# Optimization experiments

Measured on AMD Instinct MI355X. Metric: run time of the kernel, lower is better.

## Reference

```python
import jax, jax.numpy as jnp
import numpy as np

NUM_HEADS = 8
HEAD_DIM = 64
HIDDEN = 512
ROPE_THETA = 500000.0


def _make_rope(seq_len, head_dim, theta):
    inv_freq = 1.0 / (theta ** (np.arange(0, head_dim, 2, dtype=np.float32) / head_dim))
    t = np.arange(seq_len, dtype=np.float32)
    freqs = np.outer(t, inv_freq)                  # [S, hd/2]
    emb = np.concatenate([freqs, freqs], axis=-1)  # [S, hd]
    return jnp.asarray(np.cos(emb)), jnp.asarray(np.sin(emb))


def setup_inputs() -> dict:
    key = jax.random.key(0)
    ks = jax.random.split(key, 5)
    B, S, H = 1, 4096, HIDDEN
    num_registers = 32
    hidden_states = jax.random.normal(ks[0], (B, S, H), dtype=jnp.float32)
    scale = 0.02
    Wq = jax.random.normal(ks[1], (H, H), dtype=jnp.float32) * scale
    Wk = jax.random.normal(ks[2], (H, H), dtype=jnp.float32) * scale
    Wv = jax.random.normal(ks[3], (H, H), dtype=jnp.float32) * scale
    Wo = jax.random.normal(ks[4], (H, H), dtype=jnp.float32) * scale
    cos, sin = _make_rope(S - num_registers, HEAD_DIM, ROPE_THETA)
    return {"hidden_states": hidden_states, "Wq": Wq, "Wk": Wk, "Wv": Wv,
            "Wo": Wo, "cos": cos, "sin": sin, "num_registers": num_registers}


def _rotate_half(x):
    x1, x2 = jnp.split(x, 2, axis=-1)
    return jnp.concatenate([-x2, x1], axis=-1)


def _apply_rope(q, k, cos, sin):
    # cos/sin: [S_real, hd] broadcast over [B, H, S_real, hd]
    cos = cos[None, None]
    sin = sin[None, None]
    return q * cos + _rotate_half(q) * sin, k * cos + _rotate_half(k) * sin


def reference(hidden_states, Wq, Wk, Wv, Wo, cos, sin, num_registers):
    B, S, _ = hidden_states.shape
    def proj(W):
        # torch Linear: x @ W.T -> [B, S, H] -> [B, nh, S, hd]
        y = jnp.einsum('bsh,oh->bso', hidden_states, W)
        return y.reshape(B, S, NUM_HEADS, HEAD_DIM).transpose(0, 2, 1, 3)
    q, k, v = proj(Wq), proj(Wk), proj(Wv)

    if num_registers > 0:
        q_reg, q_real = q[:, :, :num_registers], q[:, :, num_registers:]
        k_reg, k_real = k[:, :, :num_registers], k[:, :, num_registers:]
        q_real, k_real = _apply_rope(q_real, k_real, cos, sin)
        q = jnp.concatenate([q_reg, q_real], axis=2)
        k = jnp.concatenate([k_reg, k_real], axis=2)
    else:
        q, k = _apply_rope(q, k, cos, sin)

    scale = 1.0 / jnp.sqrt(jnp.float32(HEAD_DIM))
    scores = jnp.einsum('bhqd,bhkd->bhqk', q, k) * scale  # [B, nh, S, S]
    causal = jnp.tril(jnp.ones((S, S), dtype=bool))
    scores = jnp.where(causal[None, None], scores, jnp.float32(-1e30))
    attn = jax.nn.softmax(scores, axis=-1)
    out = jnp.einsum('bhqk,bhkd->bhqd', attn, v)
    out = out.transpose(0, 2, 1, 3).reshape(B, S, HIDDEN)
    return jnp.einsum('bsh,oh->bso', out, Wo)
```

## Files before the change

### kernel.cpp

```cpp
#include <hip/hip_runtime.h>
#include <cstdint>
#include <cstddef>

#define S_LEN 4096
#define HID   512
#define NHEAD 8
#define HD    64
#define SCALE_LOG2E 0.1803368801111204f

typedef __bf16 bf16;
typedef __bf16 bf16x8 __attribute__((ext_vector_type(8)));
typedef __bf16 bf16x4 __attribute__((ext_vector_type(4)));
typedef float  f32x4  __attribute__((ext_vector_type(4)));
typedef unsigned uint4v __attribute__((ext_vector_type(4)));

__global__ __launch_bounds__(256) void cvt_in(
    const float* __restrict__ hs, const float* __restrict__ wq,
    const float* __restrict__ wk, const float* __restrict__ wv,
    const float* __restrict__ wo,
    bf16* __restrict__ xb, bf16* __restrict__ wqb, bf16* __restrict__ wkb,
    bf16* __restrict__ wvb, bf16* __restrict__ wob)
{
    int e = (blockIdx.x * 256 + threadIdx.x) * 4;
    const float* s; bf16* d; int o;
    if (e < 2 * 1024 * 1024) { s = hs; d = xb; o = e; }
    else {
        int t = e - 2 * 1024 * 1024;
        int wi = t >> 18;
        o = t & ((1 << 18) - 1);
        s = (wi == 0) ? wq : (wi == 1) ? wk : (wi == 2) ? wv : wo;
        d = (wi == 0) ? wqb : (wi == 1) ? wkb : (wi == 2) ? wvb : wob;
    }
    const float4 v = *(const float4*)(s + o);
    bf16x4 ob;
    ob[0] = (bf16)v.x; ob[1] = (bf16)v.y; ob[2] = (bf16)v.z; ob[3] = (bf16)v.w;
    *(bf16x4*)(d + o) = ob;
}

__global__ __launch_bounds__(256) void gemm_qkv(
    const bf16* __restrict__ Xb,
    const bf16* __restrict__ W0, const bf16* __restrict__ W1, const bf16* __restrict__ W2,
    const float* __restrict__ cosT, const float* __restrict__ sinT,
    const int* __restrict__ nregp,
    bf16* __restrict__ Qh, bf16* __restrict__ Kh, bf16* __restrict__ Vt)
{
    const int z = blockIdx.z;
    const bf16* W = (z == 0) ? W0 : (z == 1 ? W1 : W2);
    const int m0 = blockIdx.y * 64, n0 = blockIdx.x * 128;
    __shared__ bf16 lA[64][8][8];
    __shared__ bf16 lB[128][8][8];
    __shared__ bf16 scratch[64][136];
    const int tid = threadIdx.x;
    const int lane = tid & 63, w = tid >> 6;
    const int l16 = lane & 15, lc = lane >> 4, l7 = lane & 7;
    const int wm = (w & 1) * 32, wn = (w >> 1) * 64;
    f32x4 acc[2][4] = {};

    for (int k0 = 0; k0 < HID; k0 += 64) {
        __syncthreads();
#pragma unroll
        for (int i = 0; i < 2; i++) {
            int uu = tid + 256 * i;
            int m = uu >> 3, c = uu & 7;
            *(bf16x8*)(&lA[m][c ^ (m & 7)][0]) =
                *(const bf16x8*)(Xb + (size_t)(m0 + m) * HID + k0 + 8 * c);
        }
#pragma unroll
        for (int i = 0; i < 4; i++) {
            int uu = tid + 256 * i;
            int m = uu >> 3, c = uu & 7;
            *(bf16x8*)(&lB[m][c ^ (m & 7)][0]) =
                *(const bf16x8*)(W + (size_t)(n0 + m) * HID + k0 + 8 * c);
        }
        __syncthreads();
#pragma unroll
        for (int ks = 0; ks < 2; ks++) {
            bf16x8 af[2], bfr[4];
#pragma unroll
            for (int i = 0; i < 2; i++)
                af[i]  = *(const bf16x8*)(&lA[wm + 16 * i + l16][(4 * ks + lc) ^ l7][0]);
#pragma unroll
            for (int j = 0; j < 4; j++)
                bfr[j] = *(const bf16x8*)(&lB[wn + 16 * j + l16][(4 * ks + lc) ^ l7][0]);
#pragma unroll
            for (int i = 0; i < 2; i++)
#pragma unroll
                for (int j = 0; j < 4; j++)
                    acc[i][j] = __builtin_amdgcn_mfma_f32_16x16x32_bf16(
                        af[i], bfr[j], acc[i][j], 0, 0, 0);
        }
    }

    if (z == 2) {
        const int h = (n0 + wn) >> 6;
#pragma unroll
        for (int i = 0; i < 2; i++) {
            const int s0r = m0 + wm + 16 * i + 4 * lc;
#pragma unroll
            for (int j = 0; j < 4; j++) {
                const int dl = 16 * j + l16;
                bf16x4 o;
#pragma unroll
                for (int r = 0; r < 4; r++) o[r] = (bf16)acc[i][j][r];
                *(bf16x4*)(Vt + ((size_t)(h * HD + dl)) * S_LEN + s0r) = o;
            }
        }
    } else {
        const int nreg = *nregp;
        bf16* dst = (z == 0) ? Qh : Kh;
#pragma unroll
        for (int i = 0; i < 2; i++) {
            const int sl0 = wm + 16 * i + 4 * lc;
#pragma unroll
            for (int r = 0; r < 4; r++) {
                const int s = m0 + sl0 + r;
                float c0 = 1.f, sn0 = 0.f, c1 = 1.f, sn1 = 0.f;
                if (s >= nreg) {
                    const int p = s - nreg;
                    c0  = cosT[(size_t)p * HD + l16];
                    sn0 = sinT[(size_t)p * HD + l16];
                    c1  = cosT[(size_t)p * HD + 16 + l16];
                    sn1 = sinT[(size_t)p * HD + 16 + l16];
                }
                const float x0 = acc[i][0][r], x1 = acc[i][1][r];
                const float x2 = acc[i][2][r], x3 = acc[i][3][r];
                bf16* row = &scratch[sl0 + r][wn];
                row[l16]      = (bf16)(x0 * c0 - x2 * sn0);
                row[l16 + 16] = (bf16)(x1 * c1 - x3 * sn1);
                row[l16 + 32] = (bf16)(x2 * c0 + x0 * sn0);
                row[l16 + 48] = (bf16)(x3 * c1 + x1 * sn1);
            }
        }
        __syncthreads();
        const int h0 = n0 >> 6;
#pragma unroll
        for (int i = 0; i < 4; i++) {
            int u = tid + 256 * i;
            int row = u >> 4, c = u & 15;
            bf16x8 val = *(const bf16x8*)(&scratch[row][c * 8]);
            *(bf16x8*)(dst + ((size_t)(h0 + (c >> 3)) * S_LEN + m0 + row) * HD +
                       (c & 7) * 8) = val;
        }
    }
}

__global__ __launch_bounds__(256) void gemm_out(
    const bf16* __restrict__ X, const bf16* __restrict__ Wb,
    float* __restrict__ Y)
{
    const int m0 = blockIdx.y * 64, n0 = blockIdx.x * 64;
    __shared__ bf16 lA[64][8][8];
    __shared__ bf16 lB[64][8][8];
    const int tid = threadIdx.x;
    const int lane = tid & 63, w = tid >> 6;
    const int l16 = lane & 15, lc = lane >> 4, l7 = lane & 7;
    const int wm = (w & 1) * 32, wn = (w >> 1) * 32;
    f32x4 acc[2][2] = {};

    for (int k0 = 0; k0 < HID; k0 += 64) {
        __syncthreads();
#pragma unroll
        for (int i = 0; i < 2; i++) {
            int uu = tid + 256 * i;
            int m = uu >> 3, c = uu & 7;
            *(bf16x8*)(&lA[m][c ^ (m & 7)][0]) =
                *(const bf16x8*)(X + (size_t)(m0 + m) * HID + k0 + 8 * c);
        }
#pragma unroll
        for (int i = 0; i < 2; i++) {
            int uu = tid + 256 * i;
            int m = uu >> 3, c = uu & 7;
            *(bf16x8*)(&lB[m][c ^ (m & 7)][0]) =
                *(const bf16x8*)(Wb + (size_t)(n0 + m) * HID + k0 + 8 * c);
        }
        __syncthreads();
#pragma unroll
        for (int ks = 0; ks < 2; ks++) {
            bf16x8 af[2], bfr[2];
#pragma unroll
            for (int i = 0; i < 2; i++) {
                af[i]  = *(const bf16x8*)(&lA[wm + 16 * i + l16][(4 * ks + lc) ^ l7][0]);
                bfr[i] = *(const bf16x8*)(&lB[wn + 16 * i + l16][(4 * ks + lc) ^ l7][0]);
            }
#pragma unroll
            for (int i = 0; i < 2; i++)
#pragma unroll
                for (int j = 0; j < 2; j++)
                    acc[i][j] = __builtin_amdgcn_mfma_f32_16x16x32_bf16(
                        af[i], bfr[j], acc[i][j], 0, 0, 0);
        }
    }
#pragma unroll
    for (int i = 0; i < 2; i++) {
        int row = m0 + wm + 16 * i + 4 * lc;
#pragma unroll
        for (int j = 0; j < 2; j++) {
            int col = n0 + wn + 16 * j + l16;
#pragma unroll
            for (int r = 0; r < 4; r++)
                Y[(size_t)(row + r) * HID + col] = acc[i][j][r];
        }
    }
}

__global__ __launch_bounds__(256) void attn_part(
    const bf16* __restrict__ Qh, const bf16* __restrict__ Kh,
    const bf16* __restrict__ Vt, float* __restrict__ Opart,
    float* __restrict__ Lpart)
{
    const int h = blockIdx.x >> 2;
    const int ch = blockIdx.x & 3;
    const int bt = 63 - (int)blockIdx.y;
    const int qb = bt * 64;
    const int nkt = bt + 1;
    const int k0 = (nkt * ch) >> 2;
    const int k1 = (nkt * (ch + 1)) >> 2;
    const int tid = threadIdx.x;
    const int lane = tid & 63, w = tid >> 6;
    const int l16 = lane & 15, lc = lane >> 4, l7 = lane & 7;

    float* Op = Opart + ((size_t)(h * 64 + bt) * 4 + ch) * 4096;
    float* Lp = Lpart + ((size_t)(h * 64 + bt) * 4 + ch) * 64;

    if (k0 >= k1) {
        const f32x4 z = {0.f, 0.f, 0.f, 0.f};
#pragma unroll
        for (int i = 0; i < 4; i++)
            *(f32x4*)(Op + 4 * (tid + 256 * i)) = z;
        if (tid < 64) Lp[tid] = 0.f;
        return;
    }

    __shared__ bf16 lK[64][8][8];
    __shared__ bf16 lV[64][8][8];

    const bf16* Kb_ = Kh + (size_t)h * S_LEN * HD;
    const bf16* Vb_ = Vt + (size_t)h * HD * S_LEN;

    int srow[2], scol[2];
#pragma unroll
    for (int i = 0; i < 2; i++) {
        int uu = tid + 256 * i;
        srow[i] = uu >> 3;
        scol[i] = uu & 7;
    }

    bf16x8 qf[2];
    {
        const bf16* qrow = Qh + (size_t)h * S_LEN * HD + (size_t)(qb + 16 * w + l16) * HD;
        qf[0] = *(const bf16x8*)(qrow + 8 * lc);
        qf[1] = *(const bf16x8*)(qrow + 32 + 8 * lc);
    }
    f32x4 oacc[4] = {};
    float l_sum = 0.f;

    bf16x8 kr[2], vr[2];
#pragma unroll
    for (int i = 0; i < 2; i++) {
        kr[i] = *(const bf16x8*)(Kb_ + (size_t)(k0 * 64 + srow[i]) * HD + 8 * scol[i]);
        vr[i] = *(const bf16x8*)(Vb_ + (size_t)srow[i] * S_LEN + k0 * 64 + 8 * scol[i]);
    }

    for (int kt = k0; kt < k1; kt++) {
#pragma unroll
        for (int i = 0; i < 2; i++) {
            *(bf16x8*)(&lK[srow[i]][scol[i] ^ (srow[i] & 7)][0]) = kr[i];
            *(bf16x8*)(&lV[srow[i]][scol[i] ^ (srow[i] & 7)][0]) = vr[i];
        }
        __syncthreads();

        if (kt + 1 < k1) {
#pragma unroll
            for (int i = 0; i < 2; i++) {
                kr[i] = *(const bf16x8*)(Kb_ + (size_t)((kt + 1) * 64 + srow[i]) * HD +
                                         8 * scol[i]);
                vr[i] = *(const bf16x8*)(Vb_ + (size_t)srow[i] * S_LEN +
                                         (kt + 1) * 64 + 8 * scol[i]);
            }
        }

        f32x4 sacc[4] = {};
#pragma unroll
        for (int ks = 0; ks < 2; ks++)
#pragma unroll
            for (int j = 0; j < 4; j++) {
                bf16x8 kf = *(const bf16x8*)(&lK[16 * j + l16][(4 * ks + lc) ^ l7][0]);
                sacc[j] = __builtin_amdgcn_mfma_f32_16x16x32_bf16(
                    kf, qf[ks], sacc[j], 0, 0, 0);
            }

        float pv[4][4];
#pragma unroll
        for (int j = 0; j < 4; j++)
#pragma unroll
            for (int r = 0; r < 4; r++)
                pv[j][r] = __builtin_amdgcn_exp2f(sacc[j][r] * SCALE_LOG2E);
        if (kt == nkt - 1) {
            const int qg = qb + 16 * w + l16;
#pragma unroll
            for (int j = 0; j < 4; j++)
#pragma unroll
                for (int r = 0; r < 4; r++) {
                    const int keyg = kt * 64 + 16 * j + 4 * lc + r;
                    if (keyg > qg) pv[j][r] = 0.f;
                }
        }
#pragma unroll
        for (int j = 0; j < 4; j++)
            l_sum += (pv[j][0] + pv[j][1]) + (pv[j][2] + pv[j][3]);

        unsigned wp[4][2];
#pragma unroll
        for (int j = 0; j < 4; j++) {
            asm("v_cvt_pk_bf16_f32 %0, %1, %2"
                : "=v"(wp[j][0]) : "v"(pv[j][0]), "v"(pv[j][1]));
            asm("v_cvt_pk_bf16_f32 %0, %1, %2"
                : "=v"(wp[j][1]) : "v"(pv[j][2]), "v"(pv[j][3]));
        }
        bf16x8 pb[2];
#pragma unroll
        for (int ks = 0; ks < 2; ks++) {
            uint4v ow;
#pragma unroll
            for (int u = 0; u < 2; u++) {
                unsigned a = wp[2 * ks][u], b = wp[2 * ks + 1][u];
                asm("v_permlane32_swap_b32 %0, %1" : "+v"(a), "+v"(b));
                asm("v_permlane16_swap_b32 %0, %1" : "+v"(a), "+v"(b));
                ow[u] = a;
                ow[u + 2] = b;
            }
            pb[ks] = __builtin_bit_cast(bf16x8, ow);
        }

#pragma unroll
        for (int ks = 0; ks < 2; ks++)
#pragma unroll
            for (int j = 0; j < 4; j++) {
                bf16x8 vf = *(const bf16x8*)(&lV[16 * j + l16][(4 * ks + lc) ^ l7][0]);
                oacc[j] = __builtin_amdgcn_mfma_f32_16x16x32_bf16(
                    vf, pb[ks], oacc[j], 0, 0, 0);
            }

        __syncthreads();
    }

    l_sum += __shfl_xor(l_sum, 16, 64);
    l_sum += __shfl_xor(l_sum, 32, 64);
    if (lane < 16) Lp[16 * w + l16] = l_sum;

#pragma unroll
    for (int j = 0; j < 4; j++)
        *(f32x4*)(Op + (size_t)(16 * w + l16) * 64 + 16 * j + 4 * lc) = oacc[j];
}

__global__ __launch_bounds__(256) void attn_combine(
    const float* __restrict__ Opart, const float* __restrict__ Lpart,
    bf16* __restrict__ Ob)
{
    const int h = blockIdx.x, bt = blockIdx.y;
    const size_t base = (size_t)(h * 64 + bt) * 4;
    const float* O0 = Opart + base * 4096;
    const float* L0 = Lpart + base * 64;
    const int t = threadIdx.x;
    const int q = t >> 2, dq = (t & 3) * 16;
    const float l = (L0[q] + L0[64 + q]) + (L0[128 + q] + L0[192 + q]);
    const float inv = 1.0f / l;
    bf16* out = Ob + (size_t)(bt * 64 + q) * HID + h * HD + dq;
#pragma unroll
    for (int g = 0; g < 2; g++) {
        bf16x8 o8;
#pragma unroll
        for (int e = 0; e < 2; e++) {
            const int off = q * 64 + dq + 8 * g + 4 * e;
            f32x4 a = *(const f32x4*)(O0 + off);
            f32x4 b = *(const f32x4*)(O0 + 4096 + off);
            f32x4 c = *(const f32x4*)(O0 + 8192 + off);
            f32x4 d = *(const f32x4*)(O0 + 12288 + off);
#pragma unroll
            for (int r = 0; r < 4; r++)
                o8[4 * e + r] = (bf16)(((a[r] + b[r]) + (c[r] + d[r])) * inv);
        }
        *(bf16x8*)(out + 8 * g) = o8;
    }
}

extern "C" void kernel_launch(void* const* d_in, const int* in_sizes, int n_in,
                              void* d_out, int out_size, void* d_ws, size_t ws_size,
                              hipStream_t stream) {
    const float* hs   = (const float*)d_in[0];
    const float* Wq   = (const float*)d_in[1];
    const float* Wk   = (const float*)d_in[2];
    const float* Wv   = (const float*)d_in[3];
    const float* Wo   = (const float*)d_in[4];
    const float* cosT = (const float*)d_in[5];
    const float* sinT = (const float*)d_in[6];
    const int*   nreg = (const int*)d_in[7];

    char* ws = (char*)d_ws;
    const size_t MiB = 1 << 20;
    bf16*  Qh    = (bf16*)(ws);
    bf16*  Kh    = (bf16*)(ws + 4 * MiB);
    bf16*  Vt    = (bf16*)(ws + 8 * MiB);
    bf16*  Ob    = (bf16*)(ws + 12 * MiB);
    float* Opart = (float*)(ws + 16 * MiB);
    float* Lpart = (float*)(ws + 48 * MiB);
    bf16*  Xb    = (bf16*)(ws + 49 * MiB);
    bf16*  Wqb   = (bf16*)(ws + 53 * MiB);
    bf16*  Wkb   = (bf16*)(ws + 53 * MiB + 512 * 1024);
    bf16*  Wvb   = (bf16*)(ws + 54 * MiB);
    bf16*  Wob   = (bf16*)(ws + 54 * MiB + 512 * 1024);

    cvt_in<<<3072, 256, 0, stream>>>(hs, Wq, Wk, Wv, Wo, Xb, Wqb, Wkb, Wvb, Wob);
    gemm_qkv<<<dim3(4, 64, 3), 256, 0, stream>>>(Xb, Wqb, Wkb, Wvb,
                                                 cosT, sinT, nreg, Qh, Kh, Vt);
    attn_part<<<dim3(32, 64), 256, 0, stream>>>(Qh, Kh, Vt, Opart, Lpart);
    attn_combine<<<dim3(8, 64), 256, 0, stream>>>(Opart, Lpart, Ob);
    gemm_out<<<dim3(8, 64), 256, 0, stream>>>(Ob, Wob, (float*)d_out);
}
```

Before: 132.8 us.

## Double-buffer K/V tiles in shared memory for attention partial kernel

Changes the attention partial kernel from a single LDS K/V buffer to a ping-pong pair. Each iteration stores the already-loaded next tile into the alternate buffer and issues global loads two tiles ahead, so LDS stores overlap compute on the current tile. Also adds a min-blocks-per-CU hint of 4 to launch bounds, which may cap registers. The cost is doubled LDS use (32 KB per block) and possible register pressure or spills.

```diff
diff --git a/kernel.cpp b/kernel.cpp
--- a/kernel.cpp
+++ b/kernel.cpp
@@ -203,7 +203,7 @@
     }
 }
 
-__global__ __launch_bounds__(256) void attn_part(
+__global__ __launch_bounds__(256, 4) void attn_part(
     const bf16* __restrict__ Qh, const bf16* __restrict__ Kh,
     const bf16* __restrict__ Vt, float* __restrict__ Opart,
     float* __restrict__ Lpart)
@@ -231,8 +231,8 @@
         return;
     }
 
-    __shared__ bf16 lK[64][8][8];
-    __shared__ bf16 lV[64][8][8];
+    __shared__ bf16 lK[2][64][8][8];
+    __shared__ bf16 lV[2][64][8][8];
 
     const bf16* Kb_ = Kh + (size_t)h * S_LEN * HD;
     const bf16* Vb_ = Vt + (size_t)h * HD * S_LEN;
@@ -260,22 +260,38 @@
         kr[i] = *(const bf16x8*)(Kb_ + (size_t)(k0 * 64 + srow[i]) * HD + 8 * scol[i]);
         vr[i] = *(const bf16x8*)(Vb_ + (size_t)srow[i] * S_LEN + k0 * 64 + 8 * scol[i]);
     }
-
-    for (int kt = k0; kt < k1; kt++) {
-#pragma unroll
-        for (int i = 0; i < 2; i++) {
-            *(bf16x8*)(&lK[srow[i]][scol[i] ^ (srow[i] & 7)][0]) = kr[i];
-            *(bf16x8*)(&lV[srow[i]][scol[i] ^ (srow[i] & 7)][0]) = vr[i];
-        }
-        __syncthreads();
-
+#pragma unroll
+    for (int i = 0; i < 2; i++) {
+        *(bf16x8*)(&lK[0][srow[i]][scol[i] ^ (srow[i] & 7)][0]) = kr[i];
+        *(bf16x8*)(&lV[0][srow[i]][scol[i] ^ (srow[i] & 7)][0]) = vr[i];
+    }
+    if (k0 + 1 < k1) {
+#pragma unroll
+        for (int i = 0; i < 2; i++) {
+            kr[i] = *(const bf16x8*)(Kb_ + (size_t)((k0 + 1) * 64 + srow[i]) * HD +
+                                     8 * scol[i]);
+            vr[i] = *(const bf16x8*)(Vb_ + (size_t)srow[i] * S_LEN +
+                                     (k0 + 1) * 64 + 8 * scol[i]);
+        }
+    }
+    __syncthreads();
+
+    int p = 0;
+    for (int kt = k0; kt < k1; kt++, p ^= 1) {
         if (kt + 1 < k1) {
 #pragma unroll
             for (int i = 0; i < 2; i++) {
-                kr[i] = *(const bf16x8*)(Kb_ + (size_t)((kt + 1) * 64 + srow[i]) * HD +
-                                         8 * scol[i]);
-                vr[i] = *(const bf16x8*)(Vb_ + (size_t)srow[i] * S_LEN +
-                                         (kt + 1) * 64 + 8 * scol[i]);
+                *(bf16x8*)(&lK[p ^ 1][srow[i]][scol[i] ^ (srow[i] & 7)][0]) = kr[i];
+                *(bf16x8*)(&lV[p ^ 1][srow[i]][scol[i] ^ (srow[i] & 7)][0]) = vr[i];
+            }
+            if (kt + 2 < k1) {
+#pragma unroll
+                for (int i = 0; i < 2; i++) {
+                    kr[i] = *(const bf16x8*)(Kb_ + (size_t)((kt + 2) * 64 + srow[i]) * HD +
+                                             8 * scol[i]);
+                    vr[i] = *(const bf16x8*)(Vb_ + (size_t)srow[i] * S_LEN +
+                                             (kt + 2) * 64 + 8 * scol[i]);
+                }
             }
         }
 
@@ -284,7 +300,7 @@
         for (int ks = 0; ks < 2; ks++)
 #pragma unroll
             for (int j = 0; j < 4; j++) {
-                bf16x8 kf = *(const bf16x8*)(&lK[16 * j + l16][(4 * ks + lc) ^ l7][0]);
+                bf16x8 kf = *(const bf16x8*)(&lK[p][16 * j + l16][(4 * ks + lc) ^ l7][0]);
                 sacc[j] = __builtin_amdgcn_mfma_f32_16x16x32_bf16(
                     kf, qf[ks], sacc[j], 0, 0, 0);
             }
@@ -336,7 +352,7 @@
         for (int ks = 0; ks < 2; ks++)
 #pragma unroll
             for (int j = 0; j < 4; j++) {
-                bf16x8 vf = *(const bf16x8*)(&lV[16 * j + l16][(4 * ks + lc) ^ l7][0]);
+                bf16x8 vf = *(const bf16x8*)(&lV[p][16 * j + l16][(4 * ks + lc) ^ l7][0]);
                 oacc[j] = __builtin_amdgcn_mfma_f32_16x16x32_bf16(
                     vf, pb[ks], oacc[j], 0, 0, 0);
             }
```

Result: slower. 136.1 us (+2.5%).

## Fuse split-K attention combine into attn_part via last-block atomic counter

Applied to the files above, without the earlier changes.

Removes the separate attn_combine launch. Each attention block now increments a per-(head, query-tile) atomic counter after writing its partial output and row sum. The fourth block to arrive reads all four partials and writes the normalized bf16 output. Counters are zeroed in cvt_in. This saves one kernel launch and its tail gap, at the cost of release/acquire fences, an atomic per block, and combine work serialized at the end of the last-finishing blocks.

```diff
diff --git a/kernel.cpp b/kernel.cpp
--- a/kernel.cpp
+++ b/kernel.cpp
@@ -19,8 +19,13 @@
     const float* __restrict__ wk, const float* __restrict__ wv,
     const float* __restrict__ wo,
     bf16* __restrict__ xb, bf16* __restrict__ wqb, bf16* __restrict__ wkb,
-    bf16* __restrict__ wvb, bf16* __restrict__ wob)
+    bf16* __restrict__ wvb, bf16* __restrict__ wob,
+    unsigned* __restrict__ cnt)
 {
+    if (blockIdx.x == 0) {
+        cnt[threadIdx.x] = 0u;
+        cnt[threadIdx.x + 256] = 0u;
+    }
     int e = (blockIdx.x * 256 + threadIdx.x) * 4;
     const float* s; bf16* d; int o;
     if (e < 2 * 1024 * 1024) { s = hs; d = xb; o = e; }
@@ -206,7 +211,8 @@
 __global__ __launch_bounds__(256) void attn_part(
     const bf16* __restrict__ Qh, const bf16* __restrict__ Kh,
     const bf16* __restrict__ Vt, float* __restrict__ Opart,
-    float* __restrict__ Lpart)
+    float* __restrict__ Lpart, unsigned* __restrict__ cnt,
+    bf16* __restrict__ Ob)
 {
     const int h = blockIdx.x >> 2;
     const int ch = blockIdx.x & 3;
@@ -219,6 +225,10 @@
     const int lane = tid & 63, w = tid >> 6;
     const int l16 = lane & 15, lc = lane >> 4, l7 = lane & 7;
 
+    __shared__ bf16 lK[64][8][8];
+    __shared__ bf16 lV[64][8][8];
+    __shared__ int lastf;
+
     float* Op = Opart + ((size_t)(h * 64 + bt) * 4 + ch) * 4096;
     float* Lp = Lpart + ((size_t)(h * 64 + bt) * 4 + ch) * 64;
 
@@ -228,159 +238,163 @@
         for (int i = 0; i < 4; i++)
             *(f32x4*)(Op + 4 * (tid + 256 * i)) = z;
         if (tid < 64) Lp[tid] = 0.f;
-        return;
-    }
-
-    __shared__ bf16 lK[64][8][8];
-    __shared__ bf16 lV[64][8][8];
-
-    const bf16* Kb_ = Kh + (size_t)h * S_LEN * HD;
-    const bf16* Vb_ = Vt + (size_t)h * HD * S_LEN;
-
-    int srow[2], scol[2];
-#pragma unroll
-    for (int i = 0; i < 2; i++) {
-        int uu = tid + 256 * i;
-        srow[i] = uu >> 3;
-        scol[i] = uu & 7;
-    }
-
-    bf16x8 qf[2];
+    } else {
+        const bf16* Kb_ = Kh + (size_t)h * S_LEN * HD;
+        const bf16* Vb_ = Vt + (size_t)h * HD * S_LEN;
+
+        int srow[2], scol[2];
+#pragma unroll
+        for (int i = 0; i < 2; i++) {
+            int uu = tid + 256 * i;
+            srow[i] = uu >> 3;
+            scol[i] = uu & 7;
+        }
+
+        bf16x8 qf[2];
+        {
+            const bf16* qrow = Qh + (size_t)h * S_LEN * HD +
+                               (size_t)(qb + 16 * w + l16) * HD;
+            qf[0] = *(const bf16x8*)(qrow + 8 * lc);
+            qf[1] = *(const bf16x8*)(qrow + 32 + 8 * lc);
+        }
+        f32x4 oacc[4] = {};
+        float l_sum = 0.f;
+
+        bf16x8 kr[2], vr[2];
+#pragma unroll
+        for (int i = 0; i < 2; i++) {
+            kr[i] = *(const bf16x8*)(Kb_ + (size_t)(k0 * 64 + srow[i]) * HD + 8 * scol[i]);
+            vr[i] = *(const bf16x8*)(Vb_ + (size_t)srow[i] * S_LEN + k0 * 64 + 8 * scol[i]);
+        }
+
+        for (int kt = k0; kt < k1; kt++) {
+#pragma unroll
+            for (int i = 0; i < 2; i++) {
+                *(bf16x8*)(&lK[srow[i]][scol[i] ^ (srow[i] & 7)][0]) = kr[i];
+                *(bf16x8*)(&lV[srow[i]][scol[i] ^ (srow[i] & 7)][0]) = vr[i];
+            }
+            __syncthreads();
+
+            if (kt + 1 < k1) {
+#pragma unroll
+                for (int i = 0; i < 2; i++) {
+                    kr[i] = *(const bf16x8*)(Kb_ + (size_t)((kt + 1) * 64 + srow[i]) * HD +
+                                             8 * scol[i]);
+                    vr[i] = *(const bf16x8*)(Vb_ + (size_t)srow[i] * S_LEN +
+                                             (kt + 1) * 64 + 8 * scol[i]);
+                }
+            }
+
+            f32x4 sacc[4] = {};
+#pragma unroll
+            for (int ks = 0; ks < 2; ks++)
+#pragma unroll
+                for (int j = 0; j < 4; j++) {
+                    bf16x8 kf = *(const bf16x8*)(&lK[16 * j + l16][(4 * ks + lc) ^ l7][0]);
+                    sacc[j] = __builtin_amdgcn_mfma_f32_16x16x32_bf16(
+                        kf, qf[ks], sacc[j], 0, 0, 0);
+                }
+
+            float pv[4][4];
+#pragma unroll
+            for (int j = 0; j < 4; j++)
+#pragma unroll
+                for (int r = 0; r < 4; r++)
+                    pv[j][r] = __builtin_amdgcn_exp2f(sacc[j][r] * SCALE_LOG2E);
+            if (kt == nkt - 1) {
+                const int qg = qb + 16 * w + l16;
+#pragma unroll
+                for (int j = 0; j < 4; j++)
+#pragma unroll
+                    for (int r = 0; r < 4; r++) {
+                        const int keyg = kt * 64 + 16 * j + 4 * lc + r;
+                        if (keyg > qg) pv[j][r] = 0.f;
+                    }
+            }
+#pragma unroll
+            for (int j = 0; j < 4; j++)
+                l_sum += (pv[j][0] + pv[j][1]) + (pv[j][2] + pv[j][3]);
+
+            unsigned wp[4][2];
+#pragma unroll
+            for (int j = 0; j < 4; j++) {
+                asm("v_cvt_pk_bf16_f32 %0, %1, %2"
+                    : "=v"(wp[j][0]) : "v"(pv[j][0]), "v"(pv[j][1]));
+                asm("v_cvt_pk_bf16_f32 %0, %1, %2"
+                    : "=v"(wp[j][1]) : "v"(pv[j][2]), "v"(pv[j][3]));
+            }
+            bf16x8 pb[2];
+#pragma unroll
+            for (int ks = 0; ks < 2; ks++) {
+                uint4v ow;
+#pragma unroll
+                for (int u = 0; u < 2; u++) {
+                    unsigned a = wp[2 * ks][u], b = wp[2 * ks + 1][u];
+                    asm("v_permlane32_swap_b32 %0, %1" : "+v"(a), "+v"(b));
+                    asm("v_permlane16_swap_b32 %0, %1" : "+v"(a), "+v"(b));
+                    ow[u] = a;
+                    ow[u + 2] = b;
+                }
+                pb[ks] = __builtin_bit_cast(bf16x8, ow);
+            }
+
+#pragma unroll
+            for (int ks = 0; ks < 2; ks++)
+#pragma unroll
+                for (int j = 0; j < 4; j++) {
+                    bf16x8 vf = *(const bf16x8*)(&lV[16 * j + l16][(4 * ks + lc) ^ l7][0]);
+                    oacc[j] = __builtin_amdgcn_mfma_f32_16x16x32_bf16(
+                        vf, pb[ks], oacc[j], 0, 0, 0);
+                }
+
+            __syncthreads();
+        }
+
+        l_sum += __shfl_xor(l_sum, 16, 64);
+        l_sum += __shfl_xor(l_sum, 32, 64);
+        if (lane < 16) Lp[16 * w + l16] = l_sum;
+
+#pragma unroll
+        for (int j = 0; j < 4; j++)
+            *(f32x4*)(Op + (size_t)(16 * w + l16) * 64 + 16 * j + 4 * lc) = oacc[j];
+    }
+
+    __builtin_amdgcn_fence(__ATOMIC_RELEASE, "agent");
+    __syncthreads();
+    if (tid == 0) {
+        unsigned old = __hip_atomic_fetch_add(&cnt[h * 64 + bt], 1u,
+                                              __ATOMIC_ACQ_REL,
+                                              __HIP_MEMORY_SCOPE_AGENT);
+        lastf = (old == 3u);
+    }
+    __syncthreads();
+    if (!lastf) return;
+    __builtin_amdgcn_fence(__ATOMIC_ACQUIRE, "agent");
+
     {
-        const bf16* qrow = Qh + (size_t)h * S_LEN * HD + (size_t)(qb + 16 * w + l16) * HD;
-        qf[0] = *(const bf16x8*)(qrow + 8 * lc);
-        qf[1] = *(const bf16x8*)(qrow + 32 + 8 * lc);
-    }
-    f32x4 oacc[4] = {};
-    float l_sum = 0.f;
-
-    bf16x8 kr[2], vr[2];
-#pragma unroll
-    for (int i = 0; i < 2; i++) {
-        kr[i] = *(const bf16x8*)(Kb_ + (size_t)(k0 * 64 + srow[i]) * HD + 8 * scol[i]);
-        vr[i] = *(const bf16x8*)(Vb_ + (size_t)srow[i] * S_LEN + k0 * 64 + 8 * scol[i]);
-    }
-
-    for (int kt = k0; kt < k1; kt++) {
-#pragma unroll
-        for (int i = 0; i < 2; i++) {
-            *(bf16x8*)(&lK[srow[i]][scol[i] ^ (srow[i] & 7)][0]) = kr[i];
-            *(bf16x8*)(&lV[srow[i]][scol[i] ^ (srow[i] & 7)][0]) = vr[i];
-        }
-        __syncthreads();
-
-        if (kt + 1 < k1) {
-#pragma unroll
-            for (int i = 0; i < 2; i++) {
-                kr[i] = *(const bf16x8*)(Kb_ + (size_t)((kt + 1) * 64 + srow[i]) * HD +
-                                         8 * scol[i]);
-                vr[i] = *(const bf16x8*)(Vb_ + (size_t)srow[i] * S_LEN +
-                                         (kt + 1) * 64 + 8 * scol[i]);
-            }
-        }
-
-        f32x4 sacc[4] = {};
-#pragma unroll
-        for (int ks = 0; ks < 2; ks++)
-#pragma unroll
-            for (int j = 0; j < 4; j++) {
-                bf16x8 kf = *(const bf16x8*)(&lK[16 * j + l16][(4 * ks + lc) ^ l7][0]);
-                sacc[j] = __builtin_amdgcn_mfma_f32_16x16x32_bf16(
-                    kf, qf[ks], sacc[j], 0, 0, 0);
-            }
-
-        float pv[4][4];
-#pragma unroll
-        for (int j = 0; j < 4; j++)
-#pragma unroll
-            for (int r = 0; r < 4; r++)
-                pv[j][r] = __builtin_amdgcn_exp2f(sacc[j][r] * SCALE_LOG2E);
-        if (kt == nkt - 1) {
-            const int qg = qb + 16 * w + l16;
-#pragma unroll
-            for (int j = 0; j < 4; j++)
-#pragma unroll
-                for (int r = 0; r < 4; r++) {
-                    const int keyg = kt * 64 + 16 * j + 4 * lc + r;
-                    if (keyg > qg) pv[j][r] = 0.f;
-                }
-        }
-#pragma unroll
-        for (int j = 0; j < 4; j++)
-            l_sum += (pv[j][0] + pv[j][1]) + (pv[j][2] + pv[j][3]);
-
-        unsigned wp[4][2];
-#pragma unroll
-        for (int j = 0; j < 4; j++) {
-            asm("v_cvt_pk_bf16_f32 %0, %1, %2"
-                : "=v"(wp[j][0]) : "v"(pv[j][0]), "v"(pv[j][1]));
-            asm("v_cvt_pk_bf16_f32 %0, %1, %2"
-                : "=v"(wp[j][1]) : "v"(pv[j][2]), "v"(pv[j][3]));
-        }
-        bf16x8 pb[2];
-#pragma unroll
-        for (int ks = 0; ks < 2; ks++) {
-            uint4v ow;
-#pragma unroll
-            for (int u = 0; u < 2; u++) {
-                unsigned a = wp[2 * ks][u], b = wp[2 * ks + 1][u];
-                asm("v_permlane32_swap_b32 %0, %1" : "+v"(a), "+v"(b));
-                asm("v_permlane16_swap_b32 %0, %1" : "+v"(a), "+v"(b));
-                ow[u] = a;
-                ow[u + 2] = b;
-            }
-            pb[ks] = __builtin_bit_cast(bf16x8, ow);
-        }
-
-#pragma unroll
-        for (int ks = 0; ks < 2; ks++)
-#pragma unroll
-            for (int j = 0; j < 4; j++) {
-                bf16x8 vf = *(const bf16x8*)(&lV[16 * j + l16][(4 * ks + lc) ^ l7][0]);
-                oacc[j] = __builtin_amdgcn_mfma_f32_16x16x32_bf16(
-                    vf, pb[ks], oacc[j], 0, 0, 0);
-            }
-
-        __syncthreads();
-    }
-
-    l_sum += __shfl_xor(l_sum, 16, 64);
-    l_sum += __shfl_xor(l_sum, 32, 64);
-    if (lane < 16) Lp[16 * w + l16] = l_sum;
-
-#pragma unroll
-    for (int j = 0; j < 4; j++)
-        *(f32x4*)(Op + (size_t)(16 * w + l16) * 64 + 16 * j + 4 * lc) = oacc[j];
-}
-
-__global__ __launch_bounds__(256) void attn_combine(
-    const float* __restrict__ Opart, const float* __restrict__ Lpart,
-    bf16* __restrict__ Ob)
-{
-    const int h = blockIdx.x, bt = blockIdx.y;
-    const size_t base = (size_t)(h * 64 + bt) * 4;
-    const float* O0 = Opart + base * 4096;
-    const float* L0 = Lpart + base * 64;
-    const int t = threadIdx.x;
-    const int q = t >> 2, dq = (t & 3) * 16;
-    const float l = (L0[q] + L0[64 + q]) + (L0[128 + q] + L0[192 + q]);
-    const float inv = 1.0f / l;
-    bf16* out = Ob + (size_t)(bt * 64 + q) * HID + h * HD + dq;
-#pragma unroll
-    for (int g = 0; g < 2; g++) {
-        bf16x8 o8;
-#pragma unroll
-        for (int e = 0; e < 2; e++) {
-            const int off = q * 64 + dq + 8 * g + 4 * e;
-            f32x4 a = *(const f32x4*)(O0 + off);
-            f32x4 b = *(const f32x4*)(O0 + 4096 + off);
-            f32x4 c = *(const f32x4*)(O0 + 8192 + off);
-            f32x4 d = *(const f32x4*)(O0 + 12288 + off);
-#pragma unroll
-            for (int r = 0; r < 4; r++)
-                o8[4 * e + r] = (bf16)(((a[r] + b[r]) + (c[r] + d[r])) * inv);
-        }
-        *(bf16x8*)(out + 8 * g) = o8;
+        const size_t base = (size_t)(h * 64 + bt) * 4;
+        const float* O0 = Opart + base * 4096;
+        const float* L0 = Lpart + base * 64;
+        const int q = tid >> 2, dq = (tid & 3) * 16;
+        const float lsum4 = (L0[q] + L0[64 + q]) + (L0[128 + q] + L0[192 + q]);
+        const float inv = 1.0f / lsum4;
+        bf16* out = Ob + (size_t)(bt * 64 + q) * HID + h * HD + dq;
+#pragma unroll
+        for (int g = 0; g < 2; g++) {
+            bf16x8 o8;
+#pragma unroll
+            for (int e = 0; e < 2; e++) {
+                const int off = q * 64 + dq + 8 * g + 4 * e;
+                f32x4 a = *(const f32x4*)(O0 + off);
+                f32x4 b = *(const f32x4*)(O0 + 4096 + off);
+                f32x4 c = *(const f32x4*)(O0 + 8192 + off);
+                f32x4 d = *(const f32x4*)(O0 + 12288 + off);
+#pragma unroll
+                for (int r = 0; r < 4; r++)
+                    o8[4 * e + r] = (bf16)(((a[r] + b[r]) + (c[r] + d[r])) * inv);
+            }
+            *(bf16x8*)(out + 8 * g) = o8;
+        }
     }
 }
 
@@ -404,16 +418,16 @@
     bf16*  Ob    = (bf16*)(ws + 12 * MiB);
     float* Opart = (float*)(ws + 16 * MiB);
     float* Lpart = (float*)(ws + 48 * MiB);
+    unsigned* cnt = (unsigned*)(ws + 48 * MiB + 512 * 1024);
     bf16*  Xb    = (bf16*)(ws + 49 * MiB);
     bf16*  Wqb   = (bf16*)(ws + 53 * MiB);
     bf16*  Wkb   = (bf16*)(ws + 53 * MiB + 512 * 1024);
     bf16*  Wvb   = (bf16*)(ws + 54 * MiB);
     bf16*  Wob   = (bf16*)(ws + 54 * MiB + 512 * 1024);
 
-    cvt_in<<<3072, 256, 0, stream>>>(hs, Wq, Wk, Wv, Wo, Xb, Wqb, Wkb, Wvb, Wob);
+    cvt_in<<<3072, 256, 0, stream>>>(hs, Wq, Wk, Wv, Wo, Xb, Wqb, Wkb, Wvb, Wob, cnt);
     gemm_qkv<<<dim3(4, 64, 3), 256, 0, stream>>>(Xb, Wqb, Wkb, Wvb,
                                                  cosT, sinT, nreg, Qh, Kh, Vt);
-    attn_part<<<dim3(32, 64), 256, 0, stream>>>(Qh, Kh, Vt, Opart, Lpart);
-    attn_combine<<<dim3(8, 64), 256, 0, stream>>>(Opart, Lpart, Ob);
+    attn_part<<<dim3(32, 64), 256, 0, stream>>>(Qh, Kh, Vt, Opart, Lpart, cnt, Ob);
     gemm_out<<<dim3(8, 64), 256, 0, stream>>>(Ob, Wob, (float*)d_out);
 }
```

Result: slower. 433.3 us (+226.3%).
